# Performance work log

Hardware: AMD Instinct MI355X
Metric: run time of the kernel (lower is better)

## Reference

```python
import jax, jax.numpy as jnp
import numpy as np

B, S, D, H = 4, 2048, 512, 8
HD = D // H


def setup_inputs() -> dict:
    key = jax.random.key(0)
    ks = jax.random.split(key, 12)
    x = jax.random.normal(ks[0], (B, S, D), dtype=jnp.float32)
    docking_scores = jax.random.uniform(ks[1], (B, S), dtype=jnp.float32)
    mask = jax.random.randint(ks[2], (B, S), 0, 2).astype(jnp.bool_)
    s = 0.02
    Wq = jax.random.normal(ks[3], (D, D), dtype=jnp.float32) * s
    bq = jnp.zeros((D,), dtype=jnp.float32)
    Wk = jax.random.normal(ks[4], (D, D), dtype=jnp.float32) * s
    bk = jnp.zeros((D,), dtype=jnp.float32)
    Wv = jax.random.normal(ks[5], (D, D), dtype=jnp.float32) * s
    bv = jnp.zeros((D,), dtype=jnp.float32)
    Wo = jax.random.normal(ks[6], (D, D), dtype=jnp.float32) * s
    bo = jnp.zeros((D,), dtype=jnp.float32)
    alpha = jnp.float32(0.5)
    beta = jnp.float32(0.5)
    return {"x": x, "docking_scores": docking_scores, "mask": mask,
            "Wq": Wq, "bq": bq, "Wk": Wk, "bk": bk, "Wv": Wv, "bv": bv,
            "Wo": Wo, "bo": bo, "alpha": alpha, "beta": beta}


def reference(x, docking_scores, mask, Wq, bq, Wk, bk, Wv, bv, Wo, bo, alpha, beta):
    # daa_type == ATTENTION: attention + docking-score blend (alpha unused here).
    b, s, d = x.shape
    # zero docking scores at padded positions; shape (B, S, 1)
    ds = jnp.where(mask[..., None], docking_scores[..., None], 0.0)
    def proj(W, bias):
        return (jnp.einsum('bsd,ed->bse', x, W) + bias).reshape(b, s, H, HD).transpose(0, 2, 1, 3)
    Q = proj(Wq, bq)  # (B, H, S, HD)
    K = proj(Wk, bk)
    V = proj(Wv, bv)
    scores = jnp.einsum('bhqd,bhkd->bhqk', Q, K) / jnp.sqrt(jnp.float32(HD))
    scores = jnp.where(mask[:, None, None, :], scores, -jnp.inf)  # key-padding mask
    attn = jax.nn.softmax(scores, axis=-1)  # (B, H, S, S)
    # docking blend: (B,1,S,1) broadcasts over heads and key dim (faithful to torch expand)
    attn = (1.0 - beta) * attn + beta * ds[:, None, :, :]
    ctx = jnp.einsum('bhqk,bhkd->bhqd', attn, V)
    ctx = ctx.transpose(0, 2, 1, 3).reshape(b, s, d)
    return jnp.einsum('bsd,od->bso', ctx, Wo) + bo
```

## Files before the change

kernel.cpp:

```cpp
#include <hip/hip_runtime.h>
#include <hip/hip_bf16.h>

#define B_ 4
#define S_ 2048
#define D_ 512
#define H_ 8
#define HD_ 64

typedef unsigned int uint;
typedef unsigned short ushort_t;
typedef __attribute__((ext_vector_type(4))) float f32x4;
typedef __attribute__((ext_vector_type(16))) float f32x16;
typedef __attribute__((ext_vector_type(8))) short bf16x8;

#if __has_builtin(__builtin_amdgcn_exp2f)
#define EXP2F __builtin_amdgcn_exp2f
#else
#define EXP2F exp2f
#endif

__device__ __forceinline__ float bf2f(unsigned short u){ union{uint i;float f;}c; c.i = (uint)u<<16; return c.f; }
__device__ __forceinline__ unsigned short f2bf(float f){
    __hip_bfloat16 h = __float2bfloat16(f);
    return *reinterpret_cast<unsigned short*>(&h);
}

__device__ __forceinline__ void gload16(const unsigned short* g, const ushort_t* l){
    __builtin_amdgcn_global_load_lds(
        (const __attribute__((address_space(1))) unsigned int*)g,
        (__attribute__((address_space(3))) unsigned int*)l, 16, 0, 0);
}

__global__ __launch_bounds__(256) void convert_all(
    const float* __restrict__ x,
    const float* __restrict__ Wq, const float* __restrict__ Wk,
    const float* __restrict__ Wv, const float* __restrict__ Wo,
    const int* __restrict__ mask,
    ushort_t* __restrict__ xb, ushort_t* __restrict__ Wqkvb, ushort_t* __restrict__ Wob,
    float* __restrict__ mbg)
{
    const int NX = 1048576;
    const int NW = 65536;
    const int total = NX + 4 * NW;
    for (int i = blockIdx.x * 256 + threadIdx.x; i < total; i += gridDim.x * 256) {
        const float* src; ushort_t* dst; int so, dofs;
        if (i < NX) { src = x; so = i; dst = xb; dofs = i; }
        else if (i < NX + 3 * NW) {
            int j = i - NX;
            if (j < NW)          { src = Wq; so = j; }
            else if (j < 2 * NW) { src = Wk; so = j - NW; }
            else                 { src = Wv; so = j - 2 * NW; }
            dst = Wqkvb; dofs = j;
        } else { int k = i - NX - 3 * NW; src = Wo; so = k; dst = Wob; dofs = k; }
        float4 v = ((const float4*)src)[so];
        ushort4 u;
        u.x = f2bf(v.x); u.y = f2bf(v.y); u.z = f2bf(v.z); u.w = f2bf(v.w);
        ((ushort4*)dst)[dofs] = u;
    }
    for (int i = blockIdx.x * 256 + threadIdx.x; i < 2048; i += gridDim.x * 256) {
        int4 mv = ((const int4*)mask)[i];
        float4 o;
        o.x = mv.x ? 0.f : -1e30f;
        o.y = mv.y ? 0.f : -1e30f;
        o.z = mv.z ? 0.f : -1e30f;
        o.w = mv.w ? 0.f : -1e30f;
        ((float4*)mbg)[i] = o;
    }
}

template<int MODE>
__global__ __launch_bounds__(256) void gemm_mfma(
    const ushort_t* __restrict__ A, const ushort_t* __restrict__ Bw,
    const float* __restrict__ b0, const float* __restrict__ b1, const float* __restrict__ b2,
    ushort_t* __restrict__ O0, ushort_t* __restrict__ O1, ushort_t* __restrict__ O2,
    float* __restrict__ Of)
{
    __shared__ __align__(16) unsigned char smem[34816];
    ushort_t* sA = (ushort_t*)smem;
    ushort_t* sB = sA + 8192;

    const int t = threadIdx.x, w = t >> 6, l = t & 63, g = l >> 4, c = l & 15;
    const int wm = w >> 1, wn = w & 1;
    const int row0 = blockIdx.y * 128, col0 = blockIdx.x * 128;

    const ushort_t* aSrc[4]; const ushort_t* bSrc[4];
    ushort_t* aDst[4]; ushort_t* bDst[4];
    #pragma unroll
    for (int i = 0; i < 4; ++i) {
        int cc = i * 256 + t;
        int row = cc >> 3, slot = (cc & 7) ^ (row & 7);
        aSrc[i] = A  + (size_t)(row0 + row) * 512 + slot * 8;
        bSrc[i] = Bw + (size_t)(col0 + row) * 512 + slot * 8;
        aDst[i] = sA + (i * 256 + w * 64) * 8;
        bDst[i] = sB + (i * 256 + w * 64) * 8;
    }

    f32x4 acc[4][4];
    #pragma unroll
    for (int mi = 0; mi < 4; ++mi)
        #pragma unroll
        for (int ni = 0; ni < 4; ++ni) acc[mi][ni] = (f32x4)0.f;

    for (int ks = 0; ks < 8; ++ks) {
        #pragma unroll
        for (int i = 0; i < 4; ++i) {
            gload16(aSrc[i], aDst[i]);
            gload16(bSrc[i], bDst[i]);
        }
        __syncthreads();
        #pragma unroll
        for (int kh = 0; kh < 2; ++kh) {
            bf16x8 af[4], bfv[4];
            const int sw = (((kh << 2) | g) ^ (c & 7)) << 3;
            #pragma unroll
            for (int mi = 0; mi < 4; ++mi)
                af[mi] = *(const bf16x8*)&sA[(wm * 64 + mi * 16 + c) * 64 + sw];
            #pragma unroll
            for (int ni = 0; ni < 4; ++ni)
                bfv[ni] = *(const bf16x8*)&sB[(wn * 64 + ni * 16 + c) * 64 + sw];
            #pragma unroll
            for (int mi = 0; mi < 4; ++mi)
                #pragma unroll
                for (int ni = 0; ni < 4; ++ni)
                    acc[mi][ni] = __builtin_amdgcn_mfma_f32_16x16x32_bf16(af[mi], bfv[ni], acc[mi][ni], 0, 0, 0);
        }
        #pragma unroll
        for (int i = 0; i < 4; ++i) { aSrc[i] += 64; bSrc[i] += 64; }
        __syncthreads();
    }

    if (MODE == 1) {
        #pragma unroll
        for (int mi = 0; mi < 4; ++mi)
            #pragma unroll
            for (int ni = 0; ni < 4; ++ni) {
                int n = col0 + wn * 64 + ni * 16 + c;
                float bias = b0[n];
                #pragma unroll
                for (int r = 0; r < 4; ++r)
                    Of[(size_t)(row0 + wm * 64 + mi * 16 + 4 * g + r) * 512 + n] =
                        acc[mi][ni][r] + bias;
            }
    } else {
        const int which = col0 >> 9;
        const float* bias = which == 0 ? b0 : (which == 1 ? b1 : b2);
        ushort_t (*Cl)[136] = (ushort_t(*)[136])smem;
        if (which < 2) {
            #pragma unroll
            for (int mi = 0; mi < 4; ++mi)
                #pragma unroll
                for (int ni = 0; ni < 4; ++ni) {
                    int n = wn * 64 + ni * 16 + c;
                    float bb = bias[(col0 & 511) + n];
                    #pragma unroll
                    for (int r = 0; r < 4; ++r)
                        Cl[wm * 64 + mi * 16 + 4 * g + r][n] = f2bf(acc[mi][ni][r] + bb);
                }
        } else {
            #pragma unroll
            for (int mi = 0; mi < 4; ++mi)
                #pragma unroll
                for (int ni = 0; ni < 4; ++ni) {
                    int n = wn * 64 + ni * 16 + c;
                    float bb = bias[(col0 & 511) + n];
                    #pragma unroll
                    for (int r = 0; r < 4; ++r)
                        Cl[n][wm * 64 + mi * 16 + 4 * g + r] = f2bf(acc[mi][ni][r] + bb);
                }
        }
        __syncthreads();
        const int r = t >> 1, half = t & 1;
        const int b = row0 >> 11;
        if (which < 2) {
            ushort_t* Out = which == 0 ? O0 : O1;
            int s = (row0 & 2047) + r;
            int e = (col0 & 511) + half * 64;
            int h = e >> 6;
            ushort_t* dst = Out + (((size_t)(b * 8 + h) * 2048 + s) << 6);
            #pragma unroll
            for (int j = 0; j < 8; ++j)
                *(bf16x8*)(dst + j * 8) = *(const bf16x8*)&Cl[r][half * 64 + j * 8];
        } else {
            int e = (col0 & 511) + r;
            int h = e >> 6, d = e & 63;
            int s0 = (row0 & 2047) + half * 64;
            ushort_t* dst = O2 + ((size_t)(b * 8 + h) * 64 + d) * 2048 + s0;
            #pragma unroll
            for (int j = 0; j < 8; ++j)
                *(bf16x8*)(dst + j * 8) = *(const bf16x8*)&Cl[r][half * 64 + j * 8];
        }
    }
}

__global__ __launch_bounds__(256) void vsum2(
    const __hip_bfloat16* __restrict__ Vt, float* __restrict__ Vsum)
{
    const int row = blockIdx.x * 4 + (threadIdx.x >> 6);
    const int l = threadIdx.x & 63;
    const unsigned short* p = (const unsigned short*)Vt + (size_t)row * S_;
    float s = 0.f;
    #pragma unroll
    for (int i = 0; i < 4; ++i) {
        uint4 u = *(const uint4*)(p + i * 512 + l * 8);
        s += bf2f((unsigned short)(u.x & 0xffff)) + bf2f((unsigned short)(u.x >> 16));
        s += bf2f((unsigned short)(u.y & 0xffff)) + bf2f((unsigned short)(u.y >> 16));
        s += bf2f((unsigned short)(u.z & 0xffff)) + bf2f((unsigned short)(u.z >> 16));
        s += bf2f((unsigned short)(u.w & 0xffff)) + bf2f((unsigned short)(u.w >> 16));
    }
    #pragma unroll
    for (int m = 1; m < 64; m <<= 1) s += __shfl_xor(s, m);
    if (l == 0) Vsum[row] = s;
}

__global__ __launch_bounds__(256, 1) void attn_mfma(
    const __hip_bfloat16* __restrict__ Qb, const __hip_bfloat16* __restrict__ Kb,
    const __hip_bfloat16* __restrict__ Vt, const float* __restrict__ Vsum,
    const float* __restrict__ dock, const int* __restrict__ mask,
    const float* __restrict__ mbg, const float* __restrict__ beta_p,
    ushort_t* __restrict__ ctxb)
{
    __shared__ __align__(16) unsigned char smem[36864];
    ushort_t* Kbuf = (ushort_t*)smem;
    ushort_t* Vbuf = (ushort_t*)(smem + 16384);

    const int flat = blockIdx.x;
    const int xcd = flat & 7, idx = flat >> 3;
    const int bh = ((idx >> 3) << 3) | xcd;
    const int qtile = idx & 7;
    const int b = bh >> 3, h8 = bh & 7;
    const int t = threadIdx.x, w = t >> 6, lam = t & 63;
    const int lq = lam & 31, hf = lam >> 5;
    const int q0 = qtile * 256 + w * 64;
    const float beta = beta_p[0];
    const ushort_t* Kp = (const ushort_t*)Kb + (size_t)bh * S_ * HD_;
    const ushort_t* Vp = (const ushort_t*)Vt + (size_t)bh * HD_ * S_;
    const float* mbp = mbg + b * S_;

    const int srow = t >> 2, squad = t & 3;
    const int sx = ((srow & 7) << 1) | ((srow >> 3) & 1);
    int wof[4];
    #pragma unroll
    for (int i = 0; i < 4; ++i)
        wof[i] = srow * 64 + ((((squad << 2) | i) ^ sx) << 2);

    const int xr = ((lq & 7) << 1) | ((lq >> 3) & 1);

    bf16x8 qf[2][4];
    #pragma unroll
    for (int qt2 = 0; qt2 < 2; ++qt2)
        #pragma unroll
        for (int hd = 0; hd < 4; ++hd)
            qf[qt2][hd] = *(const bf16x8*)((const ushort_t*)Qb +
                ((size_t)bh * S_ + q0 + qt2 * 32 + lq) * HD_ + hd * 16 + hf * 8);

    f32x16 cacc[2][2];
    cacc[0][0] = (f32x16)0.f; cacc[0][1] = (f32x16)0.f;
    cacc[1][0] = (f32x16)0.f; cacc[1][1] = (f32x16)0.f;
    float l_[2] = {0.f, 0.f};
    const float CSC = 0.18033688011112042f;

    {
        uint4 kg0 = *(const uint4*)(Kp + (size_t)srow * 64 + squad * 16);
        uint4 kg1 = *(const uint4*)(Kp + (size_t)srow * 64 + squad * 16 + 8);
        uint4 vg0 = *(const uint4*)(Vp + (size_t)srow * 2048 + squad * 16);
        uint4 vg1 = *(const uint4*)(Vp + (size_t)srow * 2048 + squad * 16 + 8);
        *(uint2*)(Kbuf + wof[0]) = make_uint2(kg0.x, kg0.y);
        *(uint2*)(Kbuf + wof[1]) = make_uint2(kg0.z, kg0.w);
        *(uint2*)(Kbuf + wof[2]) = make_uint2(kg1.x, kg1.y);
        *(uint2*)(Kbuf + wof[3]) = make_uint2(kg1.z, kg1.w);
        *(uint2*)(Vbuf + wof[0]) = make_uint2(vg0.x, vg0.y);
        *(uint2*)(Vbuf + wof[1]) = make_uint2(vg0.z, vg0.w);
        *(uint2*)(Vbuf + wof[2]) = make_uint2(vg1.x, vg1.y);
        *(uint2*)(Vbuf + wof[3]) = make_uint2(vg1.z, vg1.w);
    }
    __syncthreads();

    for (int k0 = 0; k0 < S_; k0 += 64) {
        const int par = (k0 >> 6) & 1;
        const ushort_t* KBp = Kbuf + par * 4096;
        const ushort_t* VBp = Vbuf + par * 4096;
        const bool pre = (k0 + 64 < S_);

        uint4 kg0, kg1, vg0, vg1;
        if (pre) {
            kg0 = *(const uint4*)(Kp + (size_t)(k0 + 64 + srow) * 64 + squad * 16);
            kg1 = *(const uint4*)(Kp + (size_t)(k0 + 64 + srow) * 64 + squad * 16 + 8);
            vg0 = *(const uint4*)(Vp + (size_t)srow * 2048 + k0 + 64 + squad * 16);
            vg1 = *(const uint4*)(Vp + (size_t)srow * 2048 + k0 + 64 + squad * 16 + 8);
        }
        float4 mb[2][4];
        #pragma unroll
        for (int kt2 = 0; kt2 < 2; ++kt2)
            #pragma unroll
            for (int qd = 0; qd < 4; ++qd)
                mb[kt2][qd] = *(const float4*)(mbp + k0 + kt2 * 32 + qd * 8 + hf * 4);

        f32x16 sacc[2][2];
        sacc[0][0] = (f32x16)0.f; sacc[0][1] = (f32x16)0.f;
        sacc[1][0] = (f32x16)0.f; sacc[1][1] = (f32x16)0.f;
        __builtin_amdgcn_s_setprio(1);
        #pragma unroll
        for (int kt2 = 0; kt2 < 2; ++kt2) {
            const ushort_t* kr = KBp + (kt2 * 32 + lq) * 64;
            #pragma unroll
            for (int hd = 0; hd < 4; ++hd) {
                uint2 lo = *(const uint2*)(kr + ((((hd << 2) | (hf << 1)) ^ xr) << 2));
                uint2 hi = *(const uint2*)(kr + ((((hd << 2) | (hf << 1) | 1) ^ xr) << 2));
                union { bf16x8 v; uint4 u; } kf;
                kf.u = make_uint4(lo.x, lo.y, hi.x, hi.y);
                sacc[0][kt2] = __builtin_amdgcn_mfma_f32_32x32x16_bf16(kf.v, qf[0][hd], sacc[0][kt2], 0, 0, 0);
                sacc[1][kt2] = __builtin_amdgcn_mfma_f32_32x32x16_bf16(kf.v, qf[1][hd], sacc[1][kt2], 0, 0, 0);
            }
        }
        __builtin_amdgcn_s_setprio(0);

        float p[2][2][16];
        #pragma unroll
        for (int qt2 = 0; qt2 < 2; ++qt2) {
            float ps = 0.f;
            #pragma unroll
            for (int kt2 = 0; kt2 < 2; ++kt2)
                #pragma unroll
                for (int qd = 0; qd < 4; ++qd) {
                    float4 m4 = mb[kt2][qd];
                    float p0 = EXP2F(fmaf(sacc[qt2][kt2][qd * 4 + 0], CSC, m4.x));
                    float p1 = EXP2F(fmaf(sacc[qt2][kt2][qd * 4 + 1], CSC, m4.y));
                    float p2 = EXP2F(fmaf(sacc[qt2][kt2][qd * 4 + 2], CSC, m4.z));
                    float p3 = EXP2F(fmaf(sacc[qt2][kt2][qd * 4 + 3], CSC, m4.w));
                    p[qt2][kt2][qd * 4 + 0] = p0; p[qt2][kt2][qd * 4 + 1] = p1;
                    p[qt2][kt2][qd * 4 + 2] = p2; p[qt2][kt2][qd * 4 + 3] = p3;
                    ps += p0 + p1 + p2 + p3;
                }
            l_[qt2] += ps;
        }

        __builtin_amdgcn_s_setprio(1);
        #pragma unroll
        for (int kt2 = 0; kt2 < 2; ++kt2)
            #pragma unroll
            for (int ks = 0; ks < 2; ++ks) {
                bf16x8 pf0, pf1;
                #pragma unroll
                for (int m = 0; m < 8; ++m) {
                    pf0[m] = (short)f2bf(p[0][kt2][ks * 8 + m]);
                    pf1[m] = (short)f2bf(p[1][kt2][ks * 8 + m]);
                }
                #pragma unroll
                for (int dt = 0; dt < 2; ++dt) {
                    const ushort_t* vr = VBp + (dt * 32 + lq) * 64;
                    uint2 lo = *(const uint2*)(vr + (((8 * kt2 + 4 * ks + hf) ^ xr) << 2));
                    uint2 hi = *(const uint2*)(vr + (((8 * kt2 + 4 * ks + 2 + hf) ^ xr) << 2));
                    union { bf16x8 v; uint4 u; } vf;
                    vf.u = make_uint4(lo.x, lo.y, hi.x, hi.y);
                    cacc[0][dt] = __builtin_amdgcn_mfma_f32_32x32x16_bf16(vf.v, pf0, cacc[0][dt], 0, 0, 0);
                    cacc[1][dt] = __builtin_amdgcn_mfma_f32_32x32x16_bf16(vf.v, pf1, cacc[1][dt], 0, 0, 0);
                }
            }
        __builtin_amdgcn_s_setprio(0);

        if (pre) {
            ushort_t* KD = Kbuf + (par ^ 1) * 4096;
            ushort_t* VD = Vbuf + (par ^ 1) * 4096;
            *(uint2*)(KD + wof[0]) = make_uint2(kg0.x, kg0.y);
            *(uint2*)(KD + wof[1]) = make_uint2(kg0.z, kg0.w);
            *(uint2*)(KD + wof[2]) = make_uint2(kg1.x, kg1.y);
            *(uint2*)(KD + wof[3]) = make_uint2(kg1.z, kg1.w);
            *(uint2*)(VD + wof[0]) = make_uint2(vg0.x, vg0.y);
            *(uint2*)(VD + wof[1]) = make_uint2(vg0.z, vg0.w);
            *(uint2*)(VD + wof[2]) = make_uint2(vg1.x, vg1.y);
            *(uint2*)(VD + wof[3]) = make_uint2(vg1.z, vg1.w);
        }
        __syncthreads();
    }

    l_[0] += __shfl_xor(l_[0], 32);
    l_[1] += __shfl_xor(l_[1], 32);

    __syncthreads();

    ushort_t* ctxl = (ushort_t*)smem;
    #pragma unroll
    for (int qt2 = 0; qt2 < 2; ++qt2) {
        const int qg = q0 + qt2 * 32 + lq;
        const float w1 = (1.f - beta) / l_[qt2];
        const float dq = (mask[b * S_ + qg] ? dock[b * S_ + qg] : 0.f) * beta;
        #pragma unroll
        for (int dt = 0; dt < 2; ++dt)
            #pragma unroll
            for (int qd = 0; qd < 4; ++qd) {
                const int d0 = dt * 32 + qd * 8 + hf * 4;
                float4 vs = *(const float4*)(Vsum + bh * 64 + d0);
                float o0 = cacc[qt2][dt][qd * 4 + 0] * w1 + dq * vs.x;
                float o1 = cacc[qt2][dt][qd * 4 + 1] * w1 + dq * vs.y;
                float o2 = cacc[qt2][dt][qd * 4 + 2] * w1 + dq * vs.z;
                float o3 = cacc[qt2][dt][qd * 4 + 3] * w1 + dq * vs.w;
                uint lo = (uint)f2bf(o0) | ((uint)f2bf(o1) << 16);
                uint hi = (uint)f2bf(o2) | ((uint)f2bf(o3) << 16);
                *(uint2*)(ctxl + (size_t)w * 4608 + (qt2 * 32 + lq) * 72 + d0) =
                    make_uint2(lo, hi);
            }
    }
    __syncthreads();
    {
        ushort_t* cp = ctxb + ((size_t)(b * 2048 + q0 + lam)) * 512 + h8 * 64;
        const ushort_t* rp = ctxl + (size_t)w * 4608 + lam * 72;
        #pragma unroll
        for (int j = 0; j < 8; ++j)
            *(bf16x8*)(cp + j * 8) = *(const bf16x8*)(rp + j * 8);
    }
}

extern "C" void kernel_launch(void* const* d_in, const int* in_sizes, int n_in,
                              void* d_out, int out_size, void* d_ws, size_t ws_size,
                              hipStream_t stream)
{
    const float* x    = (const float*)d_in[0];
    const float* dock = (const float*)d_in[1];
    const int*   mask = (const int*)d_in[2];
    const float* Wq   = (const float*)d_in[3];
    const float* bq   = (const float*)d_in[4];
    const float* Wk   = (const float*)d_in[5];
    const float* bk   = (const float*)d_in[6];
    const float* Wv   = (const float*)d_in[7];
    const float* bv   = (const float*)d_in[8];
    const float* Wo   = (const float*)d_in[9];
    const float* bo   = (const float*)d_in[10];
    const float* beta = (const float*)d_in[12];
    float* out = (float*)d_out;

    const size_t nqkv = (size_t)B_ * H_ * S_ * HD_;
    ushort_t* xb    = (ushort_t*)d_ws;
    ushort_t* Qb    = xb + nqkv;
    ushort_t* Kb    = Qb + nqkv;
    ushort_t* Vt    = Kb + nqkv;
    ushort_t* Wqkvb = Vt + nqkv;
    ushort_t* Wob   = Wqkvb + 1536 * 512;
    float*    Vsum  = (float*)(Wob + 512 * 512);
    float*    mbg   = Vsum + 2048;
    ushort_t* ctxb  = xb;

    convert_all<<<1280, 256, 0, stream>>>(x, Wq, Wk, Wv, Wo, mask, xb, Wqkvb, Wob, mbg);
    gemm_mfma<0><<<dim3(12, 64), 256, 0, stream>>>(xb, Wqkvb, bq, bk, bv, Qb, Kb, Vt, nullptr);
    vsum2<<<512, 256, 0, stream>>>((const __hip_bfloat16*)Vt, Vsum);
    attn_mfma<<<256, 256, 0, stream>>>(
        (const __hip_bfloat16*)Qb, (const __hip_bfloat16*)Kb, (const __hip_bfloat16*)Vt,
        Vsum, dock, mask, mbg, beta, ctxb);
    gemm_mfma<1><<<dim3(4, 64), 256, 0, stream>>>(ctxb, Wob, bo, nullptr, nullptr,
                                                  nullptr, nullptr, nullptr, out);
}
```

Baseline: 123.1 us.

## Halve attention query tile per block and double grid for occupancy

Each wave of the attention kernel now handles 32 query rows instead of 64, so a block covers 128 queries and the grid doubles to 512 blocks. Launch bounds allow 2 blocks per CU, and LDS shrinks to 32KB to fit. The goal is more waves to hide latency and fill all 256 CUs with more than one block each. In exchange, K/V tiles are loaded into LDS twice as often per query, and each K/V fragment read feeds one MFMA instead of two.

```diff
diff --git a/kernel.cpp b/kernel.cpp
--- a/kernel.cpp
+++ b/kernel.cpp
@@ -212,25 +212,26 @@
     if (l == 0) Vsum[row] = s;
 }
 
-__global__ __launch_bounds__(256, 1) void attn_mfma(
+__global__ __launch_bounds__(256, 2) void attn_mfma(
     const __hip_bfloat16* __restrict__ Qb, const __hip_bfloat16* __restrict__ Kb,
     const __hip_bfloat16* __restrict__ Vt, const float* __restrict__ Vsum,
     const float* __restrict__ dock, const int* __restrict__ mask,
     const float* __restrict__ mbg, const float* __restrict__ beta_p,
     ushort_t* __restrict__ ctxb)
 {
-    __shared__ __align__(16) unsigned char smem[36864];
+    __shared__ __align__(16) unsigned char smem[32768];
     ushort_t* Kbuf = (ushort_t*)smem;
     ushort_t* Vbuf = (ushort_t*)(smem + 16384);
 
     const int flat = blockIdx.x;
     const int xcd = flat & 7, idx = flat >> 3;
-    const int bh = ((idx >> 3) << 3) | xcd;
-    const int qtile = idx & 7;
+    const int bh = ((idx >> 4) << 3) | xcd;
+    const int qtile = idx & 15;
     const int b = bh >> 3, h8 = bh & 7;
     const int t = threadIdx.x, w = t >> 6, lam = t & 63;
     const int lq = lam & 31, hf = lam >> 5;
-    const int q0 = qtile * 256 + w * 64;
+    const int q0 = qtile * 128 + w * 32;
+    const int qg = q0 + lq;
     const float beta = beta_p[0];
     const ushort_t* Kp = (const ushort_t*)Kb + (size_t)bh * S_ * HD_;
     const ushort_t* Vp = (const ushort_t*)Vt + (size_t)bh * HD_ * S_;
@@ -245,18 +246,16 @@
 
     const int xr = ((lq & 7) << 1) | ((lq >> 3) & 1);
 
-    bf16x8 qf[2][4];
-    #pragma unroll
-    for (int qt2 = 0; qt2 < 2; ++qt2)
-        #pragma unroll
-        for (int hd = 0; hd < 4; ++hd)
-            qf[qt2][hd] = *(const bf16x8*)((const ushort_t*)Qb +
-                ((size_t)bh * S_ + q0 + qt2 * 32 + lq) * HD_ + hd * 16 + hf * 8);
-
-    f32x16 cacc[2][2];
-    cacc[0][0] = (f32x16)0.f; cacc[0][1] = (f32x16)0.f;
-    cacc[1][0] = (f32x16)0.f; cacc[1][1] = (f32x16)0.f;
-    float l_[2] = {0.f, 0.f};
+    bf16x8 qf[4];
+    #pragma unroll
+    for (int hd = 0; hd < 4; ++hd)
+        qf[hd] = *(const bf16x8*)((const ushort_t*)Qb +
+            ((size_t)bh * S_ + qg) * HD_ + hd * 16 + hf * 8);
+
+    f32x16 cacc[2];
+    cacc[0] = (f32x16)0.f;
+    cacc[1] = (f32x16)0.f;
+    float l_ = 0.f;
     const float CSC = 0.18033688011112042f;
 
     {
@@ -295,9 +294,9 @@
             for (int qd = 0; qd < 4; ++qd)
                 mb[kt2][qd] = *(const float4*)(mbp + k0 + kt2 * 32 + qd * 8 + hf * 4);
 
-        f32x16 sacc[2][2];
-        sacc[0][0] = (f32x16)0.f; sacc[0][1] = (f32x16)0.f;
-        sacc[1][0] = (f32x16)0.f; sacc[1][1] = (f32x16)0.f;
+        f32x16 sacc[2];
+        sacc[0] = (f32x16)0.f;
+        sacc[1] = (f32x16)0.f;
         __builtin_amdgcn_s_setprio(1);
         #pragma unroll
         for (int kt2 = 0; kt2 < 2; ++kt2) {
@@ -308,43 +307,37 @@
                 uint2 hi = *(const uint2*)(kr + ((((hd << 2) | (hf << 1) | 1) ^ xr) << 2));
                 union { bf16x8 v; uint4 u; } kf;
                 kf.u = make_uint4(lo.x, lo.y, hi.x, hi.y);
-                sacc[0][kt2] = __builtin_amdgcn_mfma_f32_32x32x16_bf16(kf.v, qf[0][hd], sacc[0][kt2], 0, 0, 0);
-                sacc[1][kt2] = __builtin_amdgcn_mfma_f32_32x32x16_bf16(kf.v, qf[1][hd], sacc[1][kt2], 0, 0, 0);
+                sacc[kt2] = __builtin_amdgcn_mfma_f32_32x32x16_bf16(kf.v, qf[hd], sacc[kt2], 0, 0, 0);
             }
         }
         __builtin_amdgcn_s_setprio(0);
 
-        float p[2][2][16];
-        #pragma unroll
-        for (int qt2 = 0; qt2 < 2; ++qt2) {
-            float ps = 0.f;
-            #pragma unroll
-            for (int kt2 = 0; kt2 < 2; ++kt2)
-                #pragma unroll
-                for (int qd = 0; qd < 4; ++qd) {
-                    float4 m4 = mb[kt2][qd];
-                    float p0 = EXP2F(fmaf(sacc[qt2][kt2][qd * 4 + 0], CSC, m4.x));
-                    float p1 = EXP2F(fmaf(sacc[qt2][kt2][qd * 4 + 1], CSC, m4.y));
-                    float p2 = EXP2F(fmaf(sacc[qt2][kt2][qd * 4 + 2], CSC, m4.z));
-                    float p3 = EXP2F(fmaf(sacc[qt2][kt2][qd * 4 + 3], CSC, m4.w));
-                    p[qt2][kt2][qd * 4 + 0] = p0; p[qt2][kt2][qd * 4 + 1] = p1;
-                    p[qt2][kt2][qd * 4 + 2] = p2; p[qt2][kt2][qd * 4 + 3] = p3;
-                    ps += p0 + p1 + p2 + p3;
-                }
-            l_[qt2] += ps;
-        }
+        float p[2][16];
+        float ps = 0.f;
+        #pragma unroll
+        for (int kt2 = 0; kt2 < 2; ++kt2)
+            #pragma unroll
+            for (int qd = 0; qd < 4; ++qd) {
+                float4 m4 = mb[kt2][qd];
+                float p0 = EXP2F(fmaf(sacc[kt2][qd * 4 + 0], CSC, m4.x));
+                float p1 = EXP2F(fmaf(sacc[kt2][qd * 4 + 1], CSC, m4.y));
+                float p2 = EXP2F(fmaf(sacc[kt2][qd * 4 + 2], CSC, m4.z));
+                float p3 = EXP2F(fmaf(sacc[kt2][qd * 4 + 3], CSC, m4.w));
+                p[kt2][qd * 4 + 0] = p0; p[kt2][qd * 4 + 1] = p1;
+                p[kt2][qd * 4 + 2] = p2; p[kt2][qd * 4 + 3] = p3;
+                ps += p0 + p1 + p2 + p3;
+            }
+        l_ += ps;
 
         __builtin_amdgcn_s_setprio(1);
         #pragma unroll
         for (int kt2 = 0; kt2 < 2; ++kt2)
             #pragma unroll
             for (int ks = 0; ks < 2; ++ks) {
-                bf16x8 pf0, pf1;
-                #pragma unroll
-                for (int m = 0; m < 8; ++m) {
-                    pf0[m] = (short)f2bf(p[0][kt2][ks * 8 + m]);
-                    pf1[m] = (short)f2bf(p[1][kt2][ks * 8 + m]);
-                }
+                bf16x8 pf;
+                #pragma unroll
+                for (int m = 0; m < 8; ++m)
+                    pf[m] = (short)f2bf(p[kt2][ks * 8 + m]);
                 #pragma unroll
                 for (int dt = 0; dt < 2; ++dt) {
                     const ushort_t* vr = VBp + (dt * 32 + lq) * 64;
@@ -352,8 +345,7 @@
                     uint2 hi = *(const uint2*)(vr + (((8 * kt2 + 4 * ks + 2 + hf) ^ xr) << 2));
                     union { bf16x8 v; uint4 u; } vf;
                     vf.u = make_uint4(lo.x, lo.y, hi.x, hi.y);
-                    cacc[0][dt] = __builtin_amdgcn_mfma_f32_32x32x16_bf16(vf.v, pf0, cacc[0][dt], 0, 0, 0);
-                    cacc[1][dt] = __builtin_amdgcn_mfma_f32_32x32x16_bf16(vf.v, pf1, cacc[1][dt], 0, 0, 0);
+                    cacc[dt] = __builtin_amdgcn_mfma_f32_32x32x16_bf16(vf.v, pf, cacc[dt], 0, 0, 0);
                 }
             }
         __builtin_amdgcn_s_setprio(0);
@@ -373,16 +365,13 @@
         __syncthreads();
     }
 
-    l_[0] += __shfl_xor(l_[0], 32);
-    l_[1] += __shfl_xor(l_[1], 32);
+    l_ += __shfl_xor(l_, 32);
 
     __syncthreads();
 
     ushort_t* ctxl = (ushort_t*)smem;
-    #pragma unroll
-    for (int qt2 = 0; qt2 < 2; ++qt2) {
-        const int qg = q0 + qt2 * 32 + lq;
-        const float w1 = (1.f - beta) / l_[qt2];
+    {
+        const float w1 = (1.f - beta) / l_;
         const float dq = (mask[b * S_ + qg] ? dock[b * S_ + qg] : 0.f) * beta;
         #pragma unroll
         for (int dt = 0; dt < 2; ++dt)
@@ -390,22 +379,22 @@
             for (int qd = 0; qd < 4; ++qd) {
                 const int d0 = dt * 32 + qd * 8 + hf * 4;
                 float4 vs = *(const float4*)(Vsum + bh * 64 + d0);
-                float o0 = cacc[qt2][dt][qd * 4 + 0] * w1 + dq * vs.x;
-                float o1 = cacc[qt2][dt][qd * 4 + 1] * w1 + dq * vs.y;
-                float o2 = cacc[qt2][dt][qd * 4 + 2] * w1 + dq * vs.z;
-                float o3 = cacc[qt2][dt][qd * 4 + 3] * w1 + dq * vs.w;
+                float o0 = cacc[dt][qd * 4 + 0] * w1 + dq * vs.x;
+                float o1 = cacc[dt][qd * 4 + 1] * w1 + dq * vs.y;
+                float o2 = cacc[dt][qd * 4 + 2] * w1 + dq * vs.z;
+                float o3 = cacc[dt][qd * 4 + 3] * w1 + dq * vs.w;
                 uint lo = (uint)f2bf(o0) | ((uint)f2bf(o1) << 16);
                 uint hi = (uint)f2bf(o2) | ((uint)f2bf(o3) << 16);
-                *(uint2*)(ctxl + (size_t)w * 4608 + (qt2 * 32 + lq) * 72 + d0) =
-                    make_uint2(lo, hi);
+                *(uint2*)(ctxl + (size_t)w * 2304 + lq * 72 + d0) = make_uint2(lo, hi);
             }
     }
     __syncthreads();
     {
-        ushort_t* cp = ctxb + ((size_t)(b * 2048 + q0 + lam)) * 512 + h8 * 64;
-        const ushort_t* rp = ctxl + (size_t)w * 4608 + lam * 72;
-        #pragma unroll
-        for (int j = 0; j < 8; ++j)
+        const int qloc = lam >> 1, half = lam & 1;
+        ushort_t* cp = ctxb + ((size_t)(b * 2048 + q0 + qloc)) * 512 + h8 * 64 + half * 32;
+        const ushort_t* rp = ctxl + (size_t)w * 2304 + qloc * 72 + half * 32;
+        #pragma unroll
+        for (int j = 0; j < 4; ++j)
             *(bf16x8*)(cp + j * 8) = *(const bf16x8*)(rp + j * 8);
     }
 }
@@ -442,7 +431,7 @@
     convert_all<<<1280, 256, 0, stream>>>(x, Wq, Wk, Wv, Wo, mask, xb, Wqkvb, Wob, mbg);
     gemm_mfma<0><<<dim3(12, 64), 256, 0, stream>>>(xb, Wqkvb, bq, bk, bv, Qb, Kb, Vt, nullptr);
     vsum2<<<512, 256, 0, stream>>>((const __hip_bfloat16*)Vt, Vsum);
-    attn_mfma<<<256, 256, 0, stream>>>(
+    attn_mfma<<<512, 256, 0, stream>>>(
         (const __hip_bfloat16*)Qb, (const __hip_bfloat16*)Kb, (const __hip_bfloat16*)Vt,
         Vsum, dock, mask, mbg, beta, ctxb);
     gemm_mfma<1><<<dim3(4, 64), 256, 0, stream>>>(ctxb, Wob, bo, nullptr, nullptr,
```

After: 108.4 us. 1.14x faster.
